# Performance work log

Hardware: AMD Instinct MI355X
Metric: run time of the kernel (lower is better)

The kernel has to match this reference:

```python
import jax, jax.numpy as jnp
import numpy as np

WS = (7, 7, 7)
NUM_HEADS = 16
DIM = 512
HEAD_DIM = DIM // NUM_HEADS
SCALE = HEAD_DIM ** (-0.5)


def _rel_index():
    # Swin-3D relative position index, computed statically with numpy.
    coords = np.stack(np.meshgrid(np.arange(WS[0]), np.arange(WS[1]), np.arange(WS[2]), indexing='ij'))
    coords = coords.reshape(3, -1)                       # [3, n]
    rel = coords[:, :, None] - coords[:, None, :]        # [3, n, n]
    rel = rel.transpose(1, 2, 0).astype(np.int64)        # [n, n, 3]
    rel[..., 0] += WS[0] - 1
    rel[..., 1] += WS[1] - 1
    rel[..., 2] += WS[2] - 1
    rel[..., 0] *= (2 * WS[1] - 1) * (2 * WS[2] - 1)
    rel[..., 1] *= 2 * WS[2] - 1
    return rel.sum(-1)                                   # [n, n]

REL_INDEX = jnp.asarray(_rel_index(), dtype=jnp.int32)


def setup_inputs() -> dict:
    key = jax.random.key(0)
    ks = jax.random.split(key, 6)
    B, nw = 2, 64
    b, n, c = B * nw, WS[0] * WS[1] * WS[2], DIM  # 128, 343, 512
    x = jax.random.normal(ks[0], (b, n, c), jnp.float32)
    q_global = jax.random.normal(ks[1], (B, 1, NUM_HEADS, n, HEAD_DIM), jnp.float32)
    mask = jax.random.normal(ks[2], (nw, n, n), jnp.float32)
    kv_w = jax.random.normal(ks[3], (2 * c, c), jnp.float32) * (c ** -0.5)
    proj_w = jax.random.normal(ks[4], (c, c), jnp.float32) * (c ** -0.5)
    proj_b = jnp.zeros((c,), jnp.float32)
    num_rel = (2 * WS[0] - 1) * (2 * WS[1] - 1) * (2 * WS[2] - 1)  # 2197
    rpb_table = jax.random.normal(ks[5], (num_rel, NUM_HEADS), jnp.float32) * 0.02
    return {"x": x, "D": 7, "H": 7, "W": 7, "mask": mask, "q_global": q_global,
            "kv_w": kv_w, "proj_w": proj_w, "proj_b": proj_b, "rpb_table": rpb_table}


def reference(x, D, H, W, mask, q_global, kv_w, proj_w, proj_b, rpb_table):
    b, n, c = x.shape
    h, hd = NUM_HEADS, c // NUM_HEADS
    B = q_global.shape[0]
    # q_global [B,1,h,n,hd] repeated over windows -> [b,h,n,hd]
    q = jnp.broadcast_to(q_global, (B, b // B, h, n, hd)).reshape(b, h, n, hd) * SCALE
    kv = (x @ kv_w.T).reshape(b, n, 2, h, hd).transpose(2, 0, 3, 1, 4)  # [2,b,h,n,hd]
    k, v = kv[0], kv[1]
    attn = jnp.einsum('bhnd,bhmd->bhnm', q, k)  # [b,h,n,n]
    bias = rpb_table[REL_INDEX[:n, :n].reshape(-1)].reshape(n, n, h).transpose(2, 0, 1)
    attn = attn + bias[None]
    nw = mask.shape[0]
    attn = (attn.reshape(b // nw, nw, h, n, n) + mask[None, :, None]).reshape(b, h, n, n)
    attn = jax.nn.softmax(attn, axis=-1)
    out = jnp.einsum('bhnm,bhmd->bhnd', attn, v).transpose(0, 2, 1, 3).reshape(b, n, c)
    return out @ proj_w.T + proj_b
```

## Files before the change

### kernel.cpp

```cpp
#include <hip/hip_runtime.h>

typedef __bf16 bf16x8 __attribute__((ext_vector_type(8)));
typedef float f32x4 __attribute__((ext_vector_type(4)));

#define MFMA16(a, b, c) __builtin_amdgcn_mfma_f32_16x16x32_bf16(a, b, c, 0, 0, 0)
#define LOG2E 1.4426950408889634f

typedef __attribute__((address_space(3))) void lds_void;
typedef __attribute__((address_space(1))) const void gbl_void;
__device__ inline void glds16(const __bf16* g, __bf16* l) {
  __builtin_amdgcn_global_load_lds((gbl_void*)g, (lds_void*)l, 16, 0, 0);
}

__device__ inline float qsum4(float v) {
  v += __shfl_xor(v, 1);
  v += __shfl_xor(v, 2);
  v += __shfl_xor(v, 4);
  v += __shfl_xor(v, 8);
  return v;
}

__global__ void cvt_scale(const float* __restrict__ src, __bf16* __restrict__ dst,
                          int n8, float scale) {
  int i = blockIdx.x * blockDim.x + threadIdx.x;
  if (i >= n8) return;
  const float4* p = (const float4*)(src + i * 8);
  float4 a = p[0], b = p[1];
  bf16x8 r;
  r[0] = (__bf16)(a.x * scale); r[1] = (__bf16)(a.y * scale);
  r[2] = (__bf16)(a.z * scale); r[3] = (__bf16)(a.w * scale);
  r[4] = (__bf16)(b.x * scale); r[5] = (__bf16)(b.y * scale);
  r[6] = (__bf16)(b.z * scale); r[7] = (__bf16)(b.w * scale);
  *(bf16x8*)(dst + i * 8) = r;
}

__global__ void pack_bias(const float* __restrict__ rpb, __bf16* __restrict__ dst) {
  int i = blockIdx.x * blockDim.x + threadIdx.x;
  if (i >= 16 * 15488) return;
  int h = i / 15488, rem = i % 15488;
  int qt = rem / 704, rem2 = rem % 704;
  int tp = rem2 >> 6, lane = rem2 & 63;
  int quad = lane >> 4, l15 = lane & 15;
  bf16x8 v;
#pragma unroll
  for (int t2 = 0; t2 < 2; t2++)
#pragma unroll
    for (int r = 0; r < 4; r++) {
      int row = qt * 16 + quad * 4 + r;
      int col = (tp * 2 + t2) * 16 + l15;
      float val = -1e30f;
      if (row < 343 && col < 343) {
        int q0 = row / 49, q1 = (row / 7) % 7, q2 = row % 7;
        int k0 = col / 49, k1 = (col / 7) % 7, k2 = col % 7;
        int idx = ((q0 - k0 + 6) * 13 + (q1 - k1 + 6)) * 13 + (q2 - k2 + 6);
        val = rpb[idx * 16 + h] * LOG2E;
      }
      v[t2 * 4 + r] = (__bf16)val;
    }
  *(bf16x8*)(dst + i * 8) = v;
}

__global__ void pack_mask(const float* __restrict__ mask, __bf16* __restrict__ dst) {
  int i = blockIdx.x * blockDim.x + threadIdx.x;
  if (i >= 64 * 15488) return;
  int w = i / 15488, rem = i % 15488;
  int qt = rem / 704, rem2 = rem % 704;
  int tp = rem2 >> 6, lane = rem2 & 63;
  int quad = lane >> 4, l15 = lane & 15;
  const float* s = mask + w * 117649;
  bf16x8 v;
#pragma unroll
  for (int t2 = 0; t2 < 2; t2++)
#pragma unroll
    for (int r = 0; r < 4; r++) {
      int row = qt * 16 + quad * 4 + r;
      int col = (tp * 2 + t2) * 16 + l15;
      float val = (row < 343 && col < 343) ? s[row * 343 + col] * LOG2E : -1e30f;
      v[t2 * 4 + r] = (__bf16)val;
    }
  *(bf16x8*)(dst + i * 8) = v;
}

template <int MODE>
__global__ void __launch_bounds__(256, 2)
gemm_async(const __bf16* __restrict__ A, const __bf16* __restrict__ B, const int K,
           void* __restrict__ out0, void* __restrict__ out1,
           const float* __restrict__ pbias) {
  __shared__ __bf16 As[128 * 32];
  __shared__ __bf16 Bs[128 * 32];
  const int tid = threadIdx.x;
  const int lane = tid & 63, wave = tid >> 6;
  const int quad = lane >> 4, l15 = lane & 15;
  const int wm = wave >> 1, wn = wave & 1;
  const int m0 = blockIdx.y * 128, n0 = blockIdx.x * 128;
  const int sr = lane >> 2, sc = (lane & 3) * 8;
  const __bf16* Ab = A + (m0 + wave * 16 + sr) * K + sc;
  const __bf16* Bb = B + (n0 + wave * 16 + sr) * K + sc;
  __bf16* Asl = As + wave * 512;
  __bf16* Bsl = Bs + wave * 512;
  f32x4 acc[4][4] = {};
  for (int k0 = 0; k0 < K; k0 += 32) {
    glds16(Ab + k0, Asl);
    glds16(Ab + 64 * K + k0, Asl + 2048);
    glds16(Bb + k0, Bsl);
    glds16(Bb + 64 * K + k0, Bsl + 2048);
    __syncthreads();
    bf16x8 af[4], bfr[4];
#pragma unroll
    for (int i = 0; i < 4; i++) {
      af[i] = *(const bf16x8*)(As + (wm * 64 + i * 16 + l15) * 32 + quad * 8);
      bfr[i] = *(const bf16x8*)(Bs + (wn * 64 + i * 16 + l15) * 32 + quad * 8);
    }
#pragma unroll
    for (int i = 0; i < 4; i++)
#pragma unroll
      for (int j = 0; j < 4; j++)
        acc[i][j] = MFMA16(af[i], bfr[j], acc[i][j]);
    __syncthreads();
  }
#pragma unroll
  for (int i = 0; i < 4; i++) {
    const int rowb = m0 + wm * 64 + i * 16 + quad * 4;
#pragma unroll
    for (int r = 0; r < 4; r++) {
      const int row = rowb + r;
      if constexpr (MODE == 0) {
        const int bb = row / 343, pos = row % 343;
#pragma unroll
        for (int j = 0; j < 4; j++) {
          const int col = n0 + wn * 64 + j * 16 + l15;
          const int two = col >> 9, hh = (col >> 5) & 15, d = col & 31;
          __bf16* dst = two ? (__bf16*)out1 : (__bf16*)out0;
          dst[((bb * 16 + hh) * 343 + pos) * 32 + d] = (__bf16)acc[i][j][r];
        }
      } else {
        float* o = (float*)out0;
#pragma unroll
        for (int j = 0; j < 4; j++) {
          const int col = n0 + wn * 64 + j * 16 + l15;
          o[row * 512 + col] = acc[i][j][r] + pbias[col];
        }
      }
    }
  }
}

__global__ void __launch_bounds__(512, 2)
attn_win(const __bf16* __restrict__ qs, const __bf16* __restrict__ kk,
         const __bf16* __restrict__ vv, const __bf16* __restrict__ bias_pk,
         const __bf16* __restrict__ mask_pk, __bf16* __restrict__ ao) {
  __shared__ __bf16 Ks[352 * 40];
  __shared__ __bf16 Vt[32 * 360];
  __shared__ __bf16 Pb[8 * 640];
  const int bh = blockIdx.x;
  const int b = bh >> 4, h = bh & 15;
  const int tid = threadIdx.x;
  const int lane = tid & 63, wave = tid >> 6;
  const int quad = lane >> 4, l15 = lane & 15;
  const __bf16* ksrc = kk + (b * 16 + h) * 10976;
  const __bf16* vsrc = vv + (b * 16 + h) * 10976;
  for (int i = tid; i < 352 * 4; i += 512) {
    const int row = i >> 2, seg = (i & 3) * 8;
    bf16x8 val;
    if (row < 343) {
      val = *(const bf16x8*)(ksrc + row * 32 + seg);
    } else {
#pragma unroll
      for (int e = 0; e < 8; e++) val[e] = (__bf16)0.f;
    }
    *(bf16x8*)(Ks + row * 40 + seg) = val;
  }
  for (int i = tid; i < 32 * 17; i += 512)
    Vt[(i / 17) * 360 + 343 + (i % 17)] = (__bf16)0.f;
  for (int i = tid; i < 10976; i += 512)
    Vt[(i & 31) * 360 + (i >> 5)] = vsrc[i];
  __syncthreads();

  const int b2 = b >> 6, w = b & 63;
  const __bf16* qbase = qs + (b2 * 16 + h) * 10976;
  const __bf16* bpk = bias_pk + h * 123904;
  const __bf16* mpk = mask_pk + w * 123904;

  for (int qt = wave; qt < 22; qt += 8) {
    const int rbase = qt * 16 + quad * 4;
    const int arow = qt * 16 + l15;
    const int arowc = arow < 343 ? arow : 342;
    bf16x8 aq = *(const bf16x8*)(qbase + arowc * 32 + quad * 8);
    const __bf16* bq = bpk + qt * 5632 + lane * 8;
    const __bf16* mq = mpk + qt * 5632 + lane * 8;
    f32x4 s[22];
#pragma unroll
    for (int tp = 0; tp < 11; tp++) {
      bf16x8 bb = *(const bf16x8*)(bq + tp * 512);
      bf16x8 mm = *(const bf16x8*)(mq + tp * 512);
#pragma unroll
      for (int t2 = 0; t2 < 2; t2++)
#pragma unroll
        for (int r = 0; r < 4; r++)
          s[2 * tp + t2][r] = (float)bb[t2 * 4 + r] + (float)mm[t2 * 4 + r];
    }
#pragma unroll
    for (int t = 0; t < 22; t++) {
      bf16x8 bk = *(const bf16x8*)(Ks + (t * 16 + l15) * 40 + quad * 8);
      s[t] = MFMA16(aq, bk, s[t]);
    }
    float lsum[4] = {0.f, 0.f, 0.f, 0.f};
#pragma unroll
    for (int t = 0; t < 22; t++)
#pragma unroll
      for (int r = 0; r < 4; r++) {
        const float p = __builtin_amdgcn_exp2f(s[t][r]);
        s[t][r] = p;
        lsum[r] += p;
      }
#pragma unroll
    for (int r = 0; r < 4; r++) lsum[r] = qsum4(lsum[r]);
    f32x4 o0 = {0.f, 0.f, 0.f, 0.f}, o1 = {0.f, 0.f, 0.f, 0.f};
    __bf16* pb = Pb + wave * 640;
#pragma unroll
    for (int c = 0; c < 11; c++) {
#pragma unroll
      for (int t2 = 0; t2 < 2; t2++)
#pragma unroll
        for (int r = 0; r < 4; r++)
          pb[(quad * 4 + r) * 40 + t2 * 16 + l15] = (__bf16)s[2 * c + t2][r];
      __threadfence_block();
      bf16x8 ap = *(const bf16x8*)(pb + l15 * 40 + quad * 8);
      bf16x8 bv0 = *(const bf16x8*)(Vt + l15 * 360 + c * 32 + quad * 8);
      bf16x8 bv1 = *(const bf16x8*)(Vt + (16 + l15) * 360 + c * 32 + quad * 8);
      o0 = MFMA16(ap, bv0, o0);
      o1 = MFMA16(ap, bv1, o1);
    }
#pragma unroll
    for (int r = 0; r < 4; r++) {
      const int row = rbase + r;
      if (row < 343) {
        const float inv = __builtin_amdgcn_rcpf(lsum[r]);
        __bf16* op = ao + (b * 343 + row) * 512 + h * 32;
        op[l15] = (__bf16)(o0[r] * inv);
        op[16 + l15] = (__bf16)(o1[r] * inv);
      }
    }
  }
}

extern "C" void kernel_launch(void* const* d_in, const int* in_sizes, int n_in,
                              void* d_out, int out_size, void* d_ws, size_t ws_size,
                              hipStream_t stream) {
  (void)in_sizes; (void)n_in; (void)out_size; (void)ws_size;
  const float* x      = (const float*)d_in[0];
  const float* mask   = (const float*)d_in[4];
  const float* qg     = (const float*)d_in[5];
  const float* kv_w   = (const float*)d_in[6];
  const float* proj_w = (const float*)d_in[7];
  const float* proj_b = (const float*)d_in[8];
  const float* rpb    = (const float*)d_in[9];

  char* ws = (char*)d_ws;
  __bf16* q_bf    = (__bf16*)(ws);
  __bf16* bias_pk = (__bf16*)(ws + 702464);
  __bf16* mask_pk = (__bf16*)(ws + 4667392);
  __bf16* kvw_b   = (__bf16*)(ws + 20527104);
  __bf16* projw_b = (__bf16*)(ws + 21575680);
  __bf16* kb      = (__bf16*)(ws + 22099968);
  __bf16* vb      = (__bf16*)(ws + 67057664);
  __bf16* xb      = (__bf16*)(ws + 112015360);
  __bf16* aob     = (__bf16*)(ws + 112015360);

  const float QSCALE = 0.17677669529663687f * LOG2E;

  cvt_scale<<<172, 256, 0, stream>>>(qg, q_bf, 43904, QSCALE);
  cvt_scale<<<10976, 256, 0, stream>>>(x, xb, 2809856, 1.f);
  cvt_scale<<<256, 256, 0, stream>>>(kv_w, kvw_b, 65536, 1.f);
  cvt_scale<<<128, 256, 0, stream>>>(proj_w, projw_b, 32768, 1.f);
  pack_bias<<<968, 256, 0, stream>>>(rpb, bias_pk);
  pack_mask<<<3872, 256, 0, stream>>>(mask, mask_pk);
  gemm_async<0><<<dim3(8, 343), 256, 0, stream>>>(xb, kvw_b, 512, kb, vb, nullptr);
  attn_win<<<2048, 512, 0, stream>>>(q_bf, kb, vb, bias_pk, mask_pk, aob);
  gemm_async<1><<<dim3(4, 343), 256, 0, stream>>>(aob, projw_b, 512, d_out, nullptr, proj_b);
}
```

Measured before the change: 443.4 us.

## Compute transposed scores so P feeds PV MFMA from registers, drop LDS staging

The attention kernel now computes S^T tiles (K as A-operand, Q as B-operand), so the exp'd probabilities land in the register layout the PV MFMA needs as its A-operand. This removes the per-wave LDS round trip and fence for P. The softmax row sums come from an extra MFMA against a ones vector instead of shuffle reductions. The loop is also restructured to iterate over key chunks outermost, handling up to three query tiles per wave together so K/V fragment loads are reused across them. Bias and mask packing are permuted to match the new layout, and V transposition uses vector loads.

```diff
diff --git a/kernel.cpp b/kernel.cpp
--- a/kernel.cpp
+++ b/kernel.cpp
@@ -1,7 +1,9 @@
 #include <hip/hip_runtime.h>
 
 typedef __bf16 bf16x8 __attribute__((ext_vector_type(8)));
+typedef __bf16 bf16x2 __attribute__((ext_vector_type(2)));
 typedef float f32x4 __attribute__((ext_vector_type(4)));
+typedef unsigned u32x4v __attribute__((ext_vector_type(4)));
 
 #define MFMA16(a, b, c) __builtin_amdgcn_mfma_f32_16x16x32_bf16(a, b, c, 0, 0, 0)
 #define LOG2E 1.4426950408889634f
@@ -12,12 +14,11 @@
   __builtin_amdgcn_global_load_lds((gbl_void*)g, (lds_void*)l, 16, 0, 0);
 }
 
-__device__ inline float qsum4(float v) {
-  v += __shfl_xor(v, 1);
-  v += __shfl_xor(v, 2);
-  v += __shfl_xor(v, 4);
-  v += __shfl_xor(v, 8);
-  return v;
+__device__ inline float blo(unsigned u) { return __builtin_bit_cast(float, u << 16); }
+__device__ inline float bhi(unsigned u) { return __builtin_bit_cast(float, u & 0xffff0000u); }
+__device__ inline unsigned pk2(float a, float b) {
+  bf16x2 t; t[0] = (__bf16)a; t[1] = (__bf16)b;
+  return __builtin_bit_cast(unsigned, t);
 }
 
 __global__ void cvt_scale(const float* __restrict__ src, __bf16* __restrict__ dst,
@@ -41,17 +42,17 @@
   int qt = rem / 704, rem2 = rem % 704;
   int tp = rem2 >> 6, lane = rem2 & 63;
   int quad = lane >> 4, l15 = lane & 15;
+  int q = qt * 16 + l15;
   bf16x8 v;
 #pragma unroll
   for (int t2 = 0; t2 < 2; t2++)
 #pragma unroll
     for (int r = 0; r < 4; r++) {
-      int row = qt * 16 + quad * 4 + r;
-      int col = (tp * 2 + t2) * 16 + l15;
+      int kc = tp * 32 + quad * 8 + t2 * 4 + r;
       float val = -1e30f;
-      if (row < 343 && col < 343) {
-        int q0 = row / 49, q1 = (row / 7) % 7, q2 = row % 7;
-        int k0 = col / 49, k1 = (col / 7) % 7, k2 = col % 7;
+      if (q < 343 && kc < 343) {
+        int q0 = q / 49, q1 = (q / 7) % 7, q2 = q % 7;
+        int k0 = kc / 49, k1 = (kc / 7) % 7, k2 = kc % 7;
         int idx = ((q0 - k0 + 6) * 13 + (q1 - k1 + 6)) * 13 + (q2 - k2 + 6);
         val = rpb[idx * 16 + h] * LOG2E;
       }
@@ -67,15 +68,15 @@
   int qt = rem / 704, rem2 = rem % 704;
   int tp = rem2 >> 6, lane = rem2 & 63;
   int quad = lane >> 4, l15 = lane & 15;
+  int q = qt * 16 + l15;
   const float* s = mask + w * 117649;
   bf16x8 v;
 #pragma unroll
   for (int t2 = 0; t2 < 2; t2++)
 #pragma unroll
     for (int r = 0; r < 4; r++) {
-      int row = qt * 16 + quad * 4 + r;
-      int col = (tp * 2 + t2) * 16 + l15;
-      float val = (row < 343 && col < 343) ? s[row * 343 + col] * LOG2E : -1e30f;
+      int kc = tp * 32 + quad * 8 + t2 * 4 + r;
+      float val = (q < 343 && kc < 343) ? s[q * 343 + kc] * LOG2E : -1e30f;
       v[t2 * 4 + r] = (__bf16)val;
     }
   *(bf16x8*)(dst + i * 8) = v;
@@ -151,7 +152,6 @@
          const __bf16* __restrict__ mask_pk, __bf16* __restrict__ ao) {
   __shared__ __bf16 Ks[352 * 40];
   __shared__ __bf16 Vt[32 * 360];
-  __shared__ __bf16 Pb[8 * 640];
   const int bh = blockIdx.x;
   const int b = bh >> 4, h = bh & 15;
   const int tid = threadIdx.x;
@@ -170,75 +170,91 @@
     }
     *(bf16x8*)(Ks + row * 40 + seg) = val;
   }
-  for (int i = tid; i < 32 * 17; i += 512)
-    Vt[(i / 17) * 360 + 343 + (i % 17)] = (__bf16)0.f;
-  for (int i = tid; i < 10976; i += 512)
-    Vt[(i & 31) * 360 + (i >> 5)] = vsrc[i];
-  __syncthreads();
+  Vt[(tid >> 4) * 360 + 343 + (tid & 15)] = (__bf16)0.f;
+  for (int i = tid; i < 1372; i += 512) {
+    const int pos = i >> 2, seg = (i & 3) * 8;
+    bf16x8 v = *(const bf16x8*)(vsrc + pos * 32 + seg);
+#pragma unroll
+    for (int e = 0; e < 8; e++) Vt[(seg + e) * 360 + pos] = v[e];
+  }
 
   const int b2 = b >> 6, w = b & 63;
   const __bf16* qbase = qs + (b2 * 16 + h) * 10976;
   const __bf16* bpk = bias_pk + h * 123904;
   const __bf16* mpk = mask_pk + w * 123904;
-
-  for (int qt = wave; qt < 22; qt += 8) {
-    const int rbase = qt * 16 + quad * 4;
+  const int nqt = (wave < 6) ? 3 : 2;
+
+  bf16x8 aq[3];
+#pragma unroll
+  for (int t = 0; t < 3; t++) {
+    int qt = wave + 8 * t; if (qt > 21) qt = 21;
     const int arow = qt * 16 + l15;
     const int arowc = arow < 343 ? arow : 342;
-    bf16x8 aq = *(const bf16x8*)(qbase + arowc * 32 + quad * 8);
-    const __bf16* bq = bpk + qt * 5632 + lane * 8;
-    const __bf16* mq = mpk + qt * 5632 + lane * 8;
-    f32x4 s[22];
-#pragma unroll
-    for (int tp = 0; tp < 11; tp++) {
-      bf16x8 bb = *(const bf16x8*)(bq + tp * 512);
-      bf16x8 mm = *(const bf16x8*)(mq + tp * 512);
-#pragma unroll
-      for (int t2 = 0; t2 < 2; t2++)
-#pragma unroll
-        for (int r = 0; r < 4; r++)
-          s[2 * tp + t2][r] = (float)bb[t2 * 4 + r] + (float)mm[t2 * 4 + r];
-    }
-#pragma unroll
-    for (int t = 0; t < 22; t++) {
-      bf16x8 bk = *(const bf16x8*)(Ks + (t * 16 + l15) * 40 + quad * 8);
-      s[t] = MFMA16(aq, bk, s[t]);
-    }
-    float lsum[4] = {0.f, 0.f, 0.f, 0.f};
-#pragma unroll
-    for (int t = 0; t < 22; t++)
+    aq[t] = *(const bf16x8*)(qbase + arowc * 32 + quad * 8);
+  }
+  bf16x8 ones;
+  {
+    const __bf16 ov = (l15 == 0) ? (__bf16)1.f : (__bf16)0.f;
+#pragma unroll
+    for (int e = 0; e < 8; e++) ones[e] = ov;
+  }
+  const int krow = (l15 >> 2) * 8 + (l15 & 3);
+  __syncthreads();
+
+  f32x4 o0[3], o1[3], o2[3];
+#pragma unroll
+  for (int t = 0; t < 3; t++)
+#pragma unroll
+    for (int r = 0; r < 4; r++) { o0[t][r] = 0.f; o1[t][r] = 0.f; o2[t][r] = 0.f; }
+
+  for (int c = 0; c < 11; c++) {
+    const bf16x8 bk0 = *(const bf16x8*)(Ks + (c * 32 + krow) * 40 + quad * 8);
+    const bf16x8 bk1 = *(const bf16x8*)(Ks + (c * 32 + krow + 4) * 40 + quad * 8);
+    const bf16x8 bv0 = *(const bf16x8*)(Vt + l15 * 360 + c * 32 + quad * 8);
+    const bf16x8 bv1 = *(const bf16x8*)(Vt + (16 + l15) * 360 + c * 32 + quad * 8);
+    const __bf16* bq = bpk + c * 512 + lane * 8;
+    const __bf16* mq = mpk + c * 512 + lane * 8;
+#pragma unroll
+    for (int t = 0; t < 3; t++) {
+      if (t >= nqt) break;
+      const int qoff = (wave + 8 * t) * 5632;
+      const uint4 bu = *(const uint4*)(bq + qoff);
+      const uint4 mu = *(const uint4*)(mq + qoff);
+      f32x4 s0, s1;
+      s0[0] = blo(bu.x) + blo(mu.x); s0[1] = bhi(bu.x) + bhi(mu.x);
+      s0[2] = blo(bu.y) + blo(mu.y); s0[3] = bhi(bu.y) + bhi(mu.y);
+      s1[0] = blo(bu.z) + blo(mu.z); s1[1] = bhi(bu.z) + bhi(mu.z);
+      s1[2] = blo(bu.w) + blo(mu.w); s1[3] = bhi(bu.w) + bhi(mu.w);
+      s0 = MFMA16(bk0, aq[t], s0);
+      s1 = MFMA16(bk1, aq[t], s1);
 #pragma unroll
       for (int r = 0; r < 4; r++) {
-        const float p = __builtin_amdgcn_exp2f(s[t][r]);
-        s[t][r] = p;
-        lsum[r] += p;
-      }
-#pragma unroll
-    for (int r = 0; r < 4; r++) lsum[r] = qsum4(lsum[r]);
-    f32x4 o0 = {0.f, 0.f, 0.f, 0.f}, o1 = {0.f, 0.f, 0.f, 0.f};
-    __bf16* pb = Pb + wave * 640;
-#pragma unroll
-    for (int c = 0; c < 11; c++) {
-#pragma unroll
-      for (int t2 = 0; t2 < 2; t2++)
-#pragma unroll
-        for (int r = 0; r < 4; r++)
-          pb[(quad * 4 + r) * 40 + t2 * 16 + l15] = (__bf16)s[2 * c + t2][r];
-      __threadfence_block();
-      bf16x8 ap = *(const bf16x8*)(pb + l15 * 40 + quad * 8);
-      bf16x8 bv0 = *(const bf16x8*)(Vt + l15 * 360 + c * 32 + quad * 8);
-      bf16x8 bv1 = *(const bf16x8*)(Vt + (16 + l15) * 360 + c * 32 + quad * 8);
-      o0 = MFMA16(ap, bv0, o0);
-      o1 = MFMA16(ap, bv1, o1);
-    }
-#pragma unroll
-    for (int r = 0; r < 4; r++) {
-      const int row = rbase + r;
+        s0[r] = __builtin_amdgcn_exp2f(s0[r]);
+        s1[r] = __builtin_amdgcn_exp2f(s1[r]);
+      }
+      u32x4v uv;
+      uv[0] = pk2(s0[0], s0[1]); uv[1] = pk2(s0[2], s0[3]);
+      uv[2] = pk2(s1[0], s1[1]); uv[3] = pk2(s1[2], s1[3]);
+      const bf16x8 ap = __builtin_bit_cast(bf16x8, uv);
+      o0[t] = MFMA16(ap, bv0, o0[t]);
+      o1[t] = MFMA16(ap, bv1, o1[t]);
+      o2[t] = MFMA16(ap, ones, o2[t]);
+    }
+  }
+
+#pragma unroll
+  for (int t = 0; t < 3; t++) {
+    if (t >= nqt) break;
+    const int qt = wave + 8 * t;
+#pragma unroll
+    for (int r = 0; r < 4; r++) {
+      const float lsum = __shfl(o2[t][r], lane & 48);
+      const float inv = __builtin_amdgcn_rcpf(lsum);
+      const int row = qt * 16 + quad * 4 + r;
       if (row < 343) {
-        const float inv = __builtin_amdgcn_rcpf(lsum[r]);
         __bf16* op = ao + (b * 343 + row) * 512 + h * 32;
-        op[l15] = (__bf16)(o0[r] * inv);
-        op[16 + l15] = (__bf16)(o1[r] * inv);
+        op[l15] = (__bf16)(o0[t][r] * inv);
+        op[16 + l15] = (__bf16)(o1[t][r] * inv);
       }
     }
   }
```

Result: faster. 414.2 us (-6.6%).
